# Optimization experiments

Hardware: AMD Instinct MI355X
Metric: run time of the kernel (lower is better)

Reference implementation:

```python
import jax, jax.numpy as jnp
import numpy as np


def _cas(N):
    # Hartley cas matrix: cos(2*pi*k*n/N) + sin(2*pi*k*n/N), shape [N, N]
    n = jnp.arange(N, dtype=jnp.float32)
    ang = 2.0 * jnp.pi * n[:, None] * n[None, :] / N
    return jnp.cos(ang) + jnp.sin(ang)


def setup_inputs() -> dict:
    key = jax.random.key(0)
    k0, k1, k2, k3, k4 = jax.random.split(key, 5)
    B, N, C = 8, 4096, 768
    nb, bs, hf = 8, 96, 1
    scale = 0.02
    return {
        "x": jax.random.normal(k0, (B, N, C), jnp.float32),
        "w1": scale * jax.random.normal(k1, (2, nb, bs, bs * hf), jnp.float32),
        "b1": scale * jax.random.normal(k2, (2, nb, bs * hf), jnp.float32),
        "w2": scale * jax.random.normal(k3, (2, nb, bs * hf, bs), jnp.float32),
        "b2": scale * jax.random.normal(k4, (2, nb, bs), jnp.float32),
    }


def reference(x, w1, b1, w2, b2):
    SPARSITY = 0.01       # sparsity_threshold (softshrink lambda)
    FRAC = 1.0            # hard_thresholding_fraction
    B, N, C = x.shape
    H = W = int(np.sqrt(N))
    nb, bs = w1.shape[1], w1.shape[2]
    bias = x

    xf = x.astype(jnp.float32).reshape(B, H, W, C)
    cas = _cas(C)  # module's dht2d transforms the LAST (channel) dim
    xr = xf @ cas  # [B,H,W,C]; imag part is exactly zero after torch.complex(x, 0)
    xr = xr.reshape(B, H, W, nb, bs)

    # kept_modes = int((N//2+1)*frac), clamped by W-dim slicing semantics
    km = min(W, int((N // 2 + 1) * FRAC))

    # block-diagonal 2-layer MLP on (real, imag) with imag input == 0
    o1r = jax.nn.relu(jnp.einsum('bhwki,kio->bhwko', xr, w1[0]) + b1[0])
    o1i = jax.nn.relu(jnp.einsum('bhwki,kio->bhwko', xr, w1[1]) + b1[1])
    o2r = (jnp.einsum('bhwko,koc->bhwkc', o1r, w2[0])
           - jnp.einsum('bhwko,koc->bhwkc', o1i, w2[1]) + b2[0])
    o2i = (jnp.einsum('bhwko,koc->bhwkc', o1i, w2[0])
           + jnp.einsum('bhwko,koc->bhwkc', o1r, w2[1]) + b2[1])

    if km < W:
        mask = (jnp.arange(W) < km)[None, None, :, None, None]
        o2r = jnp.where(mask, o2r, 0.0)
        o2i = jnp.where(mask, o2i, 0.0)

    # softshrink on stacked real/imag
    ss = lambda v: jnp.sign(v) * jnp.maximum(jnp.abs(v) - SPARSITY, 0.0)
    o2r, o2i = ss(o2r), ss(o2i)

    real = o2r.reshape(B, H, W, C)
    imag = o2i.reshape(B, H, W, C)

    # idht2d: dht2d(complex) = real@cas - imag@cas, divided by TOTAL element count
    n_tot = B * H * W * C
    out = ((real - imag) @ cas) / n_tot
    out = out.reshape(B, N, C).astype(bias.dtype)
    return out + bias
```

## Files before the change

### kernel.cpp

```cpp
#include <hip/hip_runtime.h>
#include <hip/hip_bf16.h>
#include <cstdint>
#include <cstddef>

typedef __bf16 bf8_t __attribute__((ext_vector_type(8)));
typedef __bf16 bf4_t __attribute__((ext_vector_type(4)));
typedef float  f4_t  __attribute__((ext_vector_type(4)));

#define CC 768
#define NROWS 32768
#define NTOT 25165824

__device__ __forceinline__ void gld16(const void* g, void* l) {
  __builtin_amdgcn_global_load_lds(
      (const __attribute__((address_space(1))) void*)g,
      (__attribute__((address_space(3))) void*)l, 16, 0, 0);
}

__global__ void prep_all(const float* __restrict__ x, __bf16* __restrict__ xb,
                         __bf16* __restrict__ cas,
                         const float* __restrict__ w1, __bf16* __restrict__ w1f,
                         const float* __restrict__ w2, __bf16* __restrict__ w2f)
{
  const int b = blockIdx.x;
  if (b < 24576) {
    int i = (b * 256 + threadIdx.x) * 4;
    float4 v = *(const float4*)(x + i);
    bf4_t rv;
    rv[0] = (__bf16)v.x; rv[1] = (__bf16)v.y; rv[2] = (__bf16)v.z; rv[3] = (__bf16)v.w;
    *(bf4_t*)(xb + i) = rv;
  } else if (b < 26880) {
    int idx = (b - 24576) * 256 + threadIdx.x;
    int i = idx / CC, j = idx - i * CC;
    int ij = (i * j) % CC;
    float ang = 6.283185307179586f * (float)ij / (float)CC;
    cas[idx] = (__bf16)(__cosf(ang) + __sinf(ang));
  } else if (b < 27456) {
    int f = (b - 26880) * 256 + threadIdx.x;
    int j = f & 7, lane = (f >> 3) & 63, rest = f >> 9;
    int nt = rest % 12, kt = (rest / 12) % 3, blk = rest / 36;
    int k = kt * 32 + (lane >> 4) * 8 + j;
    int o = nt * 16 + (lane & 15);
    float v = (o < 96) ? w1[(0 * 8 + blk) * 9216 + k * 96 + o]
                       : w1[(1 * 8 + blk) * 9216 + k * 96 + (o - 96)];
    w1f[f] = (__bf16)v;
  } else {
    int f = (b - 27456) * 256 + threadIdx.x;
    int j = f & 7, lane = (f >> 3) & 63, rest = f >> 9;
    int nt = rest % 12, kt = (rest / 12) % 6, blk = rest / 72;
    int i = kt * 32 + (lane >> 4) * 8 + j;
    int o = nt * 16 + (lane & 15);
    float v;
    if (o < 96) v = (i < 96) ?  w2[(0 * 8 + blk) * 9216 + i * 96 + o]
                             : -w2[(1 * 8 + blk) * 9216 + (i - 96) * 96 + o];
    else        v = (i < 96) ?  w2[(1 * 8 + blk) * 9216 + i * 96 + (o - 96)]
                             :  w2[(0 * 8 + blk) * 9216 + (i - 96) * 96 + (o - 96)];
    w2f[f] = (__bf16)v;
  }
}

__global__ __launch_bounds__(256, 3) void gemm_back(
    const __bf16* __restrict__ Zb, const __bf16* __restrict__ BT,
    float* __restrict__ Cf, const float* __restrict__ Xres, float scale)
{
  __shared__ __align__(16) char smem[49152];
  const int t = threadIdx.x;
  const int lane = t & 63, wid = t >> 6;
  const int wm = (wid >> 1) * 64, wn = (wid & 1) * 64;

  const int id = blockIdx.x;
  const int sid = (id & 7) * 192 + (id >> 3);
  const int m0 = (sid / 6) * 128, n0 = (sid % 6) * 128;

  const int q = lane >> 4, r = lane & 15;
  const __bf16* gA = Zb + (size_t)(m0 + (t >> 2)) * CC + (t & 3) * 8;
  const __bf16* gB = BT + (size_t)(n0 + (t >> 2)) * CC + (t & 3) * 8;
  const int ldsOff = (t >> 2) * 32 + (t & 3) * 8;

  auto stage = [&](int b, int tile) {
    int k0 = tile * 32;
    __bf16* lA = (__bf16*)(smem + b * 16384) + ldsOff;
    __bf16* lB = (__bf16*)(smem + b * 16384 + 8192) + ldsOff;
    gld16(gA + k0, lA);
    gld16(gA + (size_t)64 * CC + k0, lA + 64 * 32);
    gld16(gB + k0, lB);
    gld16(gB + (size_t)64 * CC + k0, lB + 64 * 32);
  };

  f4_t acc[4][4] = {};
  stage(0, 0);
  stage(1, 1);
  for (int tile = 0; tile < 24; ++tile) {
    int nt = tile + 2; if (nt > 23) nt = 23;
    stage((tile + 2) % 3, nt);
    asm volatile("s_waitcnt vmcnt(8)" ::: "memory");
    __builtin_amdgcn_s_barrier();
    const __bf16* sA = (const __bf16*)(smem + (tile % 3) * 16384);
    const __bf16* sB = sA + 8192 / 2;
    bf8_t af[4], bfr[4];
#pragma unroll
    for (int i = 0; i < 4; i++)
      af[i] = *(const bf8_t*)(sA + (wm + i * 16 + r) * 32 + q * 8);
#pragma unroll
    for (int j = 0; j < 4; j++)
      bfr[j] = *(const bf8_t*)(sB + (wn + j * 16 + r) * 32 + q * 8);
#pragma unroll
    for (int i = 0; i < 4; i++)
#pragma unroll
      for (int j = 0; j < 4; j++)
        acc[i][j] = __builtin_amdgcn_mfma_f32_16x16x32_bf16(af[i], bfr[j], acc[i][j], 0, 0, 0);
    __builtin_amdgcn_s_barrier();
  }

  float* cs = (float*)smem;
#pragma unroll
  for (int h = 0; h < 2; ++h) {
    __builtin_amdgcn_s_barrier();
    if ((wid >> 1) == h) {
#pragma unroll
      for (int i = 0; i < 4; i++)
#pragma unroll
        for (int j = 0; j < 4; j++)
#pragma unroll
          for (int rr = 0; rr < 4; rr++)
            cs[(i * 16 + q * 4 + rr) * 132 + wn + j * 16 + r] = acc[i][j][rr];
    }
    __builtin_amdgcn_s_barrier();
    const int u = t & 31, row8 = t >> 5;
#pragma unroll
    for (int p = 0; p < 8; ++p) {
      int rl = p * 8 + row8;
      size_t goff = (size_t)(m0 + h * 64 + rl) * CC + n0 + u * 4;
      f4_t xr = *(const f4_t*)(Xres + goff);
      f4_t cv = *(const f4_t*)(cs + rl * 132 + u * 4);
      f4_t o;
      o[0] = cv[0] * scale + xr[0];
      o[1] = cv[1] * scale + xr[1];
      o[2] = cv[2] * scale + xr[2];
      o[3] = cv[3] * scale + xr[3];
      *(f4_t*)(Cf + goff) = o;
    }
  }
}

__global__ __launch_bounds__(384, 3) void fused3(
    const __bf16* __restrict__ A, const __bf16* __restrict__ BT,
    const __bf16* __restrict__ w1f, const __bf16* __restrict__ w2f,
    const float* __restrict__ b1, const float* __restrict__ b2,
    __bf16* __restrict__ Z)
{
  __shared__ __align__(16) char smem[63488];
  __bf16* Hs = (__bf16*)smem;
  __bf16* vt = (__bf16*)(smem + 25600);
  __bf16* zl = (__bf16*)(smem + 51200);

  const int t = threadIdx.x, lane = t & 63, w = t >> 6;
  const int id = blockIdx.x;
  const int sid = (id & 7) * 128 + (id >> 3);
  const int cbp = sid & 3;
  const int m0 = (sid >> 2) * 128;
  const int n0 = cbp * 192;
  const int q = lane >> 4, r = lane & 15;

  const __bf16* gA  = A  + (size_t)(m0 + (t >> 2)) * CC + (t & 3) * 8;
  const __bf16* gA2 = A  + (size_t)(m0 + 96 + (t >> 2)) * CC + (t & 3) * 8;
  const __bf16* gB  = BT + (size_t)(n0 + (t >> 2)) * CC + (t & 3) * 8;
  const __bf16* gB2 = BT + (size_t)(n0 + 96 + (t >> 2)) * CC + (t & 3) * 8;

  auto stage = [&](int b, int tile) {
    int k0 = tile * 32;
    char* base = smem + b * 20480;
    gld16(gA + k0, (__bf16*)base + t * 8);
    if (t < 128) gld16(gA2 + k0, (__bf16*)base + (384 + t) * 8);
    gld16(gB + k0, (__bf16*)(base + 8192) + t * 8);
    gld16(gB2 + k0, (__bf16*)(base + 8192) + (384 + t) * 8);
  };

  f4_t acc[8][2] = {};
  stage(0, 0);
  stage(1, 1);
  for (int tile = 0; tile < 24; ++tile) {
    int nt = tile + 2; if (nt > 23) nt = 23;
    stage((tile + 2) % 3, nt);
    if (w < 2) asm volatile("s_waitcnt vmcnt(8)" ::: "memory");
    else       asm volatile("s_waitcnt vmcnt(6)" ::: "memory");
    __builtin_amdgcn_s_barrier();
    const __bf16* sA = (const __bf16*)(smem + (tile % 3) * 20480);
    const __bf16* sB = (const __bf16*)(smem + (tile % 3) * 20480 + 8192);
    bf8_t af[8], bfr[2];
#pragma unroll
    for (int i = 0; i < 8; i++)
      af[i] = *(const bf8_t*)(sA + (i * 16 + r) * 32 + q * 8);
#pragma unroll
    for (int j = 0; j < 2; j++)
      bfr[j] = *(const bf8_t*)(sB + (w * 32 + j * 16 + r) * 32 + q * 8);
#pragma unroll
    for (int i = 0; i < 8; i++)
#pragma unroll
      for (int j = 0; j < 2; j++)
        acc[i][j] = __builtin_amdgcn_mfma_f32_16x16x32_bf16(af[i], bfr[j], acc[i][j], 0, 0, 0);
    __builtin_amdgcn_s_barrier();
  }
  asm volatile("s_waitcnt vmcnt(0)" ::: "memory");
  __builtin_amdgcn_s_barrier();

#pragma unroll
  for (int h = 0; h < 2; h++) {
#pragma unroll
    for (int ii = 0; ii < 4; ii++)
#pragma unroll
      for (int j = 0; j < 2; j++) {
        int col = w * 32 + j * 16 + r;
#pragma unroll
        for (int rr = 0; rr < 4; rr++) {
          int row = ii * 16 + q * 4 + rr;
          vt[row * 200 + col] = (__bf16)acc[h * 4 + ii][j][rr];
        }
      }
    __syncthreads();

#pragma unroll
    for (int cb = 0; cb < 2; cb++) {
      const int bidx = cbp * 2 + cb;
      const __bf16* w1b = w1f + (size_t)bidx * (36 * 64 * 8);
      const __bf16* w2b = w2f + (size_t)bidx * (72 * 64 * 8);
      bf8_t w1r[3][2], w2r[6][2];
#pragma unroll
      for (int kt = 0; kt < 3; kt++)
#pragma unroll
        for (int j = 0; j < 2; j++)
          w1r[kt][j] = *(const bf8_t*)(w1b + ((size_t)(kt * 12 + 2 * w + j) * 64 + lane) * 8);
#pragma unroll
      for (int kt = 0; kt < 6; kt++) {
        w2r[kt][0] = *(const bf8_t*)(w2b + ((size_t)(kt * 12 + w) * 64 + lane) * 8);
        w2r[kt][1] = *(const bf8_t*)(w2b + ((size_t)(kt * 12 + w + 6) * 64 + lane) * 8);
      }
      float bb[2];
#pragma unroll
      for (int j = 0; j < 2; j++) {
        int c = (2 * w + j) * 16 + r;
        bb[j] = (c < 96) ? b1[bidx * 96 + c] : b1[768 + bidx * 96 + (c - 96)];
      }
      const float br = b2[bidx * 96 + w * 16 + r];
      const float bi = b2[768 + bidx * 96 + w * 16 + r];

#pragma unroll
      for (int rt = 0; rt < 4; rt++) {
        const __bf16* vp = vt + (rt * 16 + r) * 200 + cb * 96 + q * 8;
        f4_t a0 = {}, a1 = {};
#pragma unroll
        for (int kt = 0; kt < 3; kt++) {
          bf8_t a = *(const bf8_t*)(vp + kt * 32);
          a0 = __builtin_amdgcn_mfma_f32_16x16x32_bf16(a, w1r[kt][0], a0, 0, 0, 0);
          a1 = __builtin_amdgcn_mfma_f32_16x16x32_bf16(a, w1r[kt][1], a1, 0, 0, 0);
        }
#pragma unroll
        for (int j = 0; j < 2; j++) {
          int c = (2 * w + j) * 16 + r;
          f4_t* ap = j ? &a1 : &a0;
#pragma unroll
          for (int rr = 0; rr < 4; rr++) {
            float v = (*ap)[rr] + bb[j];
            Hs[(rt * 16 + q * 4 + rr) * 200 + c] = (__bf16)(v > 0.f ? v : 0.f);
          }
        }
      }
      __syncthreads();
#pragma unroll
      for (int rt = 0; rt < 4; rt++) {
        f4_t ar = {}, ai = {};
#pragma unroll
        for (int kt = 0; kt < 6; kt++) {
          bf8_t a = *(const bf8_t*)(&Hs[(rt * 16 + r) * 200 + kt * 32 + q * 8]);
          ar = __builtin_amdgcn_mfma_f32_16x16x32_bf16(a, w2r[kt][0], ar, 0, 0, 0);
          ai = __builtin_amdgcn_mfma_f32_16x16x32_bf16(a, w2r[kt][1], ai, 0, 0, 0);
        }
#pragma unroll
        for (int rr = 0; rr < 4; rr++) {
          float yr = ar[rr] + br, yi = ai[rr] + bi;
          float sr = fabsf(yr) - 0.01f; sr = sr > 0.f ? copysignf(sr, yr) : 0.f;
          float si = fabsf(yi) - 0.01f; si = si > 0.f ? copysignf(si, yi) : 0.f;
          zl[(rt * 16 + q * 4 + rr) * 96 + w * 16 + r] = (__bf16)(sr - si);
        }
      }
      __syncthreads();
      {
        const uint32_t* zsrc = (const uint32_t*)zl;
        int cdw = t % 48, crow = t / 48;
        int rbase = m0 + h * 64;
#pragma unroll
        for (int it = 0; it < 8; it++) {
          int row = it * 8 + crow;
          uint32_t* dst = (uint32_t*)(Z + (size_t)(rbase + row) * CC + n0 + cb * 96);
          dst[cdw] = zsrc[row * 48 + cdw];
        }
      }
    }
  }
}


extern "C" void kernel_launch(void* const* d_in, const int* in_sizes, int n_in,
                              void* d_out, int out_size, void* d_ws, size_t ws_size,
                              hipStream_t stream) {
  const float* x  = (const float*)d_in[0];
  const float* w1 = (const float*)d_in[1];
  const float* b1 = (const float*)d_in[2];
  const float* w2 = (const float*)d_in[3];
  const float* b2 = (const float*)d_in[4];
  float* out = (float*)d_out;

  char* ws = (char*)d_ws;
  size_t off = 0;
  auto alloc = [&](size_t bytes) {
    char* p = ws + off;
    off += (bytes + 255) & ~(size_t)255;
    return p;
  };
  __bf16* casb = (__bf16*)alloc((size_t)CC * CC * 2);
  __bf16* w1f  = (__bf16*)alloc((size_t)8 * 36 * 64 * 8 * 2);
  __bf16* w2f  = (__bf16*)alloc((size_t)8 * 72 * 64 * 8 * 2);
  __bf16* xb   = (__bf16*)alloc((size_t)NTOT * 2);
  __bf16* vv   = (__bf16*)alloc((size_t)NTOT * 2);

  prep_all<<<28608, 256, 0, stream>>>(x, xb, casb, w1, w1f, w2, w2f);

  fused3<<<1024, 384, 0, stream>>>(xb, casb, w1f, w2f, b1, b2, vv);
  gemm_back<<<1536, 256, 0, stream>>>(vv, casb, out, x, 1.0f / 25165824.0f);
}
```

Measured before the change: 335.1 us.

## Shrink fused kernel LDS via split A/B buffering and per-block staging of vt

Splits the K-loop staging so A tiles keep triple buffering while B tiles use double buffering with a one-tile lookahead, and stages only the current 96-column block of the GEMM output into LDS instead of both. Together these cut shared memory from about 62KB to 50KB per workgroup so more blocks can be resident per CU. The cost is a shorter prefetch distance for B and an extra barrier per column block in the epilogue, and the LDS regions are now reused more tightly (vt overlapping the B buffers), which needs correct synchronization.

New measurement: 416.6 us. +24.3%, slower.

```diff
diff --git a/kernel.cpp b/kernel.cpp
--- a/kernel.cpp
+++ b/kernel.cpp
@@ -143,16 +143,16 @@
   }
 }
 
-__global__ __launch_bounds__(384, 3) void fused3(
+__global__ __launch_bounds__(384, 3) void fused7(
     const __bf16* __restrict__ A, const __bf16* __restrict__ BT,
     const __bf16* __restrict__ w1f, const __bf16* __restrict__ w2f,
     const float* __restrict__ b1, const float* __restrict__ b2,
     __bf16* __restrict__ Z)
 {
-  __shared__ __align__(16) char smem[63488];
+  __shared__ __align__(16) char smem[51200];
   __bf16* Hs = (__bf16*)smem;
   __bf16* vt = (__bf16*)(smem + 25600);
-  __bf16* zl = (__bf16*)(smem + 51200);
+  __bf16* zl = (__bf16*)(smem + 38912);
 
   const int t = threadIdx.x, lane = t & 63, w = t >> 6;
   const int id = blockIdx.x;
@@ -167,26 +167,33 @@
   const __bf16* gB  = BT + (size_t)(n0 + (t >> 2)) * CC + (t & 3) * 8;
   const __bf16* gB2 = BT + (size_t)(n0 + 96 + (t >> 2)) * CC + (t & 3) * 8;
 
-  auto stage = [&](int b, int tile) {
+  auto stageA = [&](int b, int tile) {
     int k0 = tile * 32;
-    char* base = smem + b * 20480;
+    char* base = smem + b * 8192;
     gld16(gA + k0, (__bf16*)base + t * 8);
     if (t < 128) gld16(gA2 + k0, (__bf16*)base + (384 + t) * 8);
-    gld16(gB + k0, (__bf16*)(base + 8192) + t * 8);
-    gld16(gB2 + k0, (__bf16*)(base + 8192) + (384 + t) * 8);
   };
+  auto stageB = [&](int b, int tile) {
+    int k0 = tile * 32;
+    char* base = smem + 24576 + b * 12288;
+    gld16(gB + k0, (__bf16*)base + t * 8);
+    gld16(gB2 + k0, (__bf16*)base + (384 + t) * 8);
+  };
 
   f4_t acc[8][2] = {};
-  stage(0, 0);
-  stage(1, 1);
+  stageB(0, 0);
+  stageA(0, 0);
+  stageA(1, 1);
   for (int tile = 0; tile < 24; ++tile) {
-    int nt = tile + 2; if (nt > 23) nt = 23;
-    stage((tile + 2) % 3, nt);
-    if (w < 2) asm volatile("s_waitcnt vmcnt(8)" ::: "memory");
-    else       asm volatile("s_waitcnt vmcnt(6)" ::: "memory");
-    __builtin_amdgcn_s_barrier();
-    const __bf16* sA = (const __bf16*)(smem + (tile % 3) * 20480);
-    const __bf16* sB = (const __bf16*)(smem + (tile % 3) * 20480 + 8192);
+    int bn = tile + 1; if (bn > 23) bn = 23;
+    int an = tile + 2; if (an > 23) an = 23;
+    stageB((tile + 1) & 1, bn);
+    stageA((tile + 2) % 3, an);
+    if (w < 2) asm volatile("s_waitcnt vmcnt(6)" ::: "memory");
+    else       asm volatile("s_waitcnt vmcnt(4)" ::: "memory");
+    __builtin_amdgcn_s_barrier();
+    const __bf16* sA = (const __bf16*)(smem + (tile % 3) * 8192);
+    const __bf16* sB = (const __bf16*)(smem + 24576 + (tile & 1) * 12288);
     bf8_t af[8], bfr[2];
 #pragma unroll
     for (int i = 0; i < 8; i++)
@@ -207,20 +214,23 @@
 #pragma unroll
   for (int h = 0; h < 2; h++) {
 #pragma unroll
-    for (int ii = 0; ii < 4; ii++)
-#pragma unroll
-      for (int j = 0; j < 2; j++) {
-        int col = w * 32 + j * 16 + r;
-#pragma unroll
-        for (int rr = 0; rr < 4; rr++) {
-          int row = ii * 16 + q * 4 + rr;
-          vt[row * 200 + col] = (__bf16)acc[h * 4 + ii][j][rr];
-        }
-      }
-    __syncthreads();
-
-#pragma unroll
     for (int cb = 0; cb < 2; cb++) {
+      if ((w / 3) == cb) {
+        const int wl = w - cb * 3;
+#pragma unroll
+        for (int ii = 0; ii < 4; ii++)
+#pragma unroll
+          for (int j = 0; j < 2; j++) {
+            int col = wl * 32 + j * 16 + r;
+#pragma unroll
+            for (int rr = 0; rr < 4; rr++) {
+              int row = ii * 16 + q * 4 + rr;
+              vt[row * 104 + col] = (__bf16)acc[h * 4 + ii][j][rr];
+            }
+          }
+      }
+      __syncthreads();
+
       const int bidx = cbp * 2 + cb;
       const __bf16* w1b = w1f + (size_t)bidx * (36 * 64 * 8);
       const __bf16* w2b = w2f + (size_t)bidx * (72 * 64 * 8);
@@ -246,7 +256,7 @@
 
 #pragma unroll
       for (int rt = 0; rt < 4; rt++) {
-        const __bf16* vp = vt + (rt * 16 + r) * 200 + cb * 96 + q * 8;
+        const __bf16* vp = vt + (rt * 16 + r) * 104 + q * 8;
         f4_t a0 = {}, a1 = {};
 #pragma unroll
         for (int kt = 0; kt < 3; kt++) {
@@ -325,6 +335,6 @@
 
   prep_all<<<28608, 256, 0, stream>>>(x, xb, casb, w1, w1f, w2, w2f);
 
-  fused3<<<1024, 384, 0, stream>>>(xb, casb, w1f, w2f, b1, b2, vv);
+  fused7<<<1024, 384, 0, stream>>>(xb, casb, w1f, w2f, b1, b2, vv);
   gemm_back<<<1536, 256, 0, stream>>>(vv, casb, out, x, 1.0f / 25165824.0f);
 }
```
